# Optimization experiments

Hardware: AMD Instinct MI355X
Metric: run time of the kernel (lower is better)

The kernel has to match this reference:

```python
import jax, jax.numpy as jnp
import numpy as np

# Dims: P patterns, L pattern length, D word dim, V vocab, H mlp hidden, C classes, N doc length
P, L, D, V, H, C, N = 256, 6, 300, 100000, 256, 5, 4096


def setup_inputs() -> dict:
    key = jax.random.key(0)
    ks = jax.random.split(key, 10)
    doc = jax.random.randint(ks[0], (N,), 0, V)
    emb = jax.random.normal(ks[1], (V, D), dtype=jnp.float32)
    diags = jax.random.normal(ks[2], (P * 2 * L, D), dtype=jnp.float32)
    diags = diags / jnp.linalg.norm(diags, axis=1, keepdims=True)  # normalize() at init
    bias = jax.random.normal(ks[3], (P * 2 * L, 1), dtype=jnp.float32)
    epsilon = jax.random.normal(ks[4], (P, L - 1), dtype=jnp.float32)
    w0 = jax.random.normal(ks[5], (H, P), dtype=jnp.float32) * 0.05
    b0 = jnp.zeros((H,), jnp.float32)
    w1 = jax.random.normal(ks[6], (H, H), dtype=jnp.float32) * 0.05
    b1 = jnp.zeros((H,), jnp.float32)
    w2 = jax.random.normal(ks[7], (C, H), dtype=jnp.float32) * 0.05
    b2 = jnp.zeros((C,), jnp.float32)
    return dict(doc=doc, emb=emb, diags=diags, bias=bias, epsilon=epsilon,
                w0=w0, b0=b0, w1=w1, b1=b1, w2=w2, b2=b2)


def reference(doc, emb, diags, bias, epsilon, w0, b0, w1, b1, w2, b2):
    # fixed scalar gates: epsilon_scale = self_loop_scale = 0.5 (non-trainable)
    sls = jax.nn.sigmoid(jnp.float32(0.5))
    eps_val = jax.nn.sigmoid(jnp.float32(0.5)) * jax.nn.sigmoid(epsilon)  # [P, L-1]

    # precompute all per-token transition matrices in one GEMM
    x = emb[doc]                                                # [N, D]
    T = jax.nn.sigmoid(x @ diags.T + bias[:, 0])                # [N, P*2*L]
    T = T.reshape(-1, P, 2, L)                                  # [N, P, 2, L]

    h0 = jnp.zeros((P, L), jnp.float32).at[:, 0].set(1.0)
    zero_pad = jnp.zeros((P, 1), jnp.float32)
    one_pad = jnp.ones((P, 1), jnp.float32)

    def step(h, Tt):  # transition_once, fused over tokens via scan
        main = jnp.concatenate([zero_pad, h[:, :-1] * Tt[:, 1, :-1]], axis=1) \
               + sls * h * Tt[:, 0, :]
        h2 = main + jnp.concatenate([one_pad, main[:, :-1] * eps_val], axis=1)
        return h2, h2[:, -1]

    _, last_states = jax.lax.scan(step, h0, T)                  # last_states: [N, P]
    scores = last_states.sum(axis=0)                            # [P]

    # MLP (num_mlp_layers=2 hidden ReLU layers, then linear to classes)
    z = scores[None, :]                                         # [1, P]
    z = jax.nn.relu(z @ w0.T + b0)
    z = jax.nn.relu(z @ w1.T + b1)
    return z @ w2.T + b2                                        # [1, C]
```

## Files before the change

kernel.cpp:

```cpp
#include <hip/hip_runtime.h>
#include <hip/hip_bf16.h>
#include <cstdint>
#include <cstddef>

#define P_ 256
#define L_ 6
#define D_ 300
#define J_ 3072
#define N_ 4096
#define H_ 256
#define C_ 5
#define KP 320
#define KSTEPS 10

#define SLS 0.62245933120185459f

typedef __attribute__((ext_vector_type(8))) short short8v;
typedef __attribute__((ext_vector_type(4))) short short4v;
typedef __attribute__((ext_vector_type(4))) float f32x4;

__device__ __forceinline__ float sigmoidf_(float x) { return 1.0f / (1.0f + __expf(-x)); }
__device__ __forceinline__ float bf2f(short s) { return __uint_as_float(((unsigned)(unsigned short)s) << 16); }

__global__ __launch_bounds__(256) void prep_XB(
    const int* __restrict__ doc, const float* __restrict__ emb,
    const float* __restrict__ diags,
    __hip_bfloat16* __restrict__ X, __hip_bfloat16* __restrict__ Bb)
{
    const int i = blockIdx.x * 256 + threadIdx.x;
    const int NX = N_ * KP;
    if (i < NX) {
        const int n = i / KP, k = i - n * KP;
        float v = (k < D_) ? emb[(size_t)doc[n] * D_ + k] : 0.0f;
        X[i] = __float2bfloat16(v);
    } else {
        const int ii = i - NX;
        const int j = ii / KP, k = ii - j * KP;
        float v = (k < D_) ? diags[(size_t)j * D_ + k] : 0.0f;
        Bb[ii] = __float2bfloat16(v);
    }
}

__global__ __launch_bounds__(256) void gemm_mfma(
    const __hip_bfloat16* __restrict__ X, const __hip_bfloat16* __restrict__ Bb,
    const float* __restrict__ bias, __hip_bfloat16* __restrict__ Tt)
{
    __shared__ __hip_bfloat16 As[2][128 * 32];
    __shared__ __hip_bfloat16 Bs[2][128 * 32];

    const int tid  = threadIdx.x;
    const int lane = tid & 63;
    const int w    = tid >> 6;
    const int wr   = w >> 1, wc = w & 1;

    const int bid = blockIdx.x;
    const int swz = (bid & 7) * 96 + (bid >> 3);
    const int bx  = swz % 24, by = swz / 24;
    const int m0  = by * 128;
    const int j0  = bx * 128;

    const int srow = w * 32 + (lane >> 2);
    const int scol = (lane & 3) * 8;

    f32x4 acc[4][4];
    #pragma unroll
    for (int m = 0; m < 4; ++m)
        #pragma unroll
        for (int n = 0; n < 4; ++n)
            acc[m][n] = (f32x4){0.f, 0.f, 0.f, 0.f};

    const int fr = lane & 15;
    const int kg = (lane >> 4) * 8;

    auto stage = [&](int kt, int b) {
        const int k0 = kt * 32;
        #pragma unroll
        for (int q = 0; q < 2; ++q) {
            const __hip_bfloat16* ga = X + (size_t)(m0 + srow + q * 16) * KP + k0 + scol;
            __builtin_amdgcn_global_load_lds(
                (const __attribute__((address_space(1))) unsigned*)ga,
                (__attribute__((address_space(3))) unsigned*)(&As[b][(w * 2 + q) * 512]),
                16, 0, 0);
            const __hip_bfloat16* gb = Bb + (size_t)(j0 + srow + q * 16) * KP + k0 + scol;
            __builtin_amdgcn_global_load_lds(
                (const __attribute__((address_space(1))) unsigned*)gb,
                (__attribute__((address_space(3))) unsigned*)(&Bs[b][(w * 2 + q) * 512]),
                16, 0, 0);
        }
    };

    stage(0, 0);
    __syncthreads();

    int buf = 0;
    for (int kt = 0; kt < KSTEPS; ++kt) {
        if (kt + 1 < KSTEPS) stage(kt + 1, buf ^ 1);

        short8v a[4], b[4];
        #pragma unroll
        for (int m = 0; m < 4; ++m)
            a[m] = *(const short8v*)(&As[buf][(wr * 64 + m * 16 + fr) * 32 + kg]);
        #pragma unroll
        for (int n = 0; n < 4; ++n)
            b[n] = *(const short8v*)(&Bs[buf][(wc * 64 + n * 16 + fr) * 32 + kg]);
        #pragma unroll
        for (int m = 0; m < 4; ++m)
            #pragma unroll
            for (int n = 0; n < 4; ++n)
                acc[m][n] = __builtin_amdgcn_mfma_f32_16x16x32_bf16(a[m], b[n], acc[m][n], 0, 0, 0);

        __syncthreads();
        buf ^= 1;
    }

    #pragma unroll
    for (int n = 0; n < 4; ++n) {
        const int j = j0 + wc * 64 + n * 16 + fr;
        const float bj = bias[j];
        #pragma unroll
        for (int m = 0; m < 4; ++m) {
            const int rbase = m0 + wr * 64 + m * 16 + (lane >> 4) * 4;
            short4v pk;
            #pragma unroll
            for (int r = 0; r < 4; ++r) {
                float v = acc[m][n][r] + bj;
                __hip_bfloat16 hb = __float2bfloat16(sigmoidf_(v));
                pk[r] = *reinterpret_cast<const short*>(&hb);
            }
            *(short4v*)(Tt + (size_t)j * N_ + rbase) = pk;
        }
    }
}

__device__ __forceinline__ void compose_maps(const float* C, const float* R, float* N)
{
    #pragma unroll
    for (int j = 0; j < 7; ++j) {
        #pragma unroll
        for (int i = 0; i < 6; ++i) {
            float a = (j == 6) ? C[42 + i] : 0.0f;
            #pragma unroll
            for (int u = 0; u < 6; ++u) a = fmaf(C[u * 7 + i], R[j * 7 + u], a);
            N[j * 7 + i] = a;
        }
        float sa = R[j * 7 + 6] + ((j == 6) ? C[48] : 0.0f);
        #pragma unroll
        for (int u = 0; u < 6; ++u) sa = fmaf(C[u * 7 + 6], R[j * 7 + u], sa);
        N[j * 7 + 6] = sa;
    }
}

__global__ __launch_bounds__(256) void scan_tree(
    const __hip_bfloat16* __restrict__ Tt, const float* __restrict__ epsilon,
    float* __restrict__ scores)
{
    __shared__ float lds[256 * 49];
    const int tid = threadIdx.x;
    const int p   = blockIdx.x;

    {
        const int c = tid;
        float ep[5];
        #pragma unroll
        for (int l = 0; l < 5; ++l)
            ep[l] = SLS * (1.0f / (1.0f + __expf(-epsilon[p * 5 + l])));

        float hc[7][6], sc[7];
        #pragma unroll
        for (int j = 0; j < 7; ++j) {
            sc[j] = 0.0f;
            #pragma unroll
            for (int i = 0; i < 6; ++i) hc[j][i] = (i == j) ? 1.0f : 0.0f;
        }

        #pragma unroll
        for (int h = 0; h < 2; ++h) {
            short8v v[12];
            #pragma unroll
            for (int l = 0; l < 12; ++l)
                v[l] = *(const short8v*)(Tt + (size_t)(p * 12 + l) * N_ + c * 16 + h * 8);

            #pragma unroll
            for (int tt = 0; tt < 8; ++tt) {
                float sT0[6], T1v[6];
                #pragma unroll
                for (int l = 0; l < 6; ++l) {
                    sT0[l] = SLS * bf2f(v[l][tt]);
                    T1v[l] = bf2f(v[6 + l][tt]);
                }
                #pragma unroll
                for (int j = 0; j < 7; ++j) {
                    float m[6];
                    m[0] = hc[j][0] * sT0[0];
                    #pragma unroll
                    for (int i = 1; i < 6; ++i)
                        m[i] = fmaf(hc[j][i - 1], T1v[i - 1], hc[j][i] * sT0[i]);
                    hc[j][0] = m[0] + ((j == 6) ? 1.0f : 0.0f);
                    #pragma unroll
                    for (int i = 1; i < 6; ++i)
                        hc[j][i] = fmaf(m[i - 1], ep[i - 1], m[i]);
                    sc[j] += hc[j][5];
                }
            }
        }

        #pragma unroll
        for (int j = 0; j < 7; ++j) {
            #pragma unroll
            for (int i = 0; i < 6; ++i) lds[c * 49 + j * 7 + i] = hc[j][i];
            lds[c * 49 + j * 7 + 6] = sc[j];
        }
    }

    for (int act = 128; act >= 1; act >>= 1) {
        __syncthreads();
        float Nn[49];
        const bool on = (tid < act);
        if (on) compose_maps(&lds[(2 * tid + 1) * 49], &lds[(2 * tid) * 49], Nn);
        __syncthreads();
        if (on) {
            #pragma unroll
            for (int q = 0; q < 49; ++q) lds[tid * 49 + q] = Nn[q];
        }
    }

    if (tid == 0) scores[p] = lds[6] + lds[48];
}

__global__ __launch_bounds__(256) void mlp_head(
    const float* __restrict__ scores,
    const float* __restrict__ w0, const float* __restrict__ b0,
    const float* __restrict__ w1, const float* __restrict__ b1,
    const float* __restrict__ w2, const float* __restrict__ b2,
    float* __restrict__ out)
{
    __shared__ float s0[H_], z0[H_], z1[H_];
    const int tid = threadIdx.x;

    s0[tid] = scores[tid];
    __syncthreads();

    float acc = b0[tid];
    {
        const float4* wr = (const float4*)(w0 + (size_t)tid * P_);
        #pragma unroll 4
        for (int q = 0; q < P_ / 4; ++q) {
            float4 w = wr[q];
            acc = fmaf(w.x, s0[q * 4 + 0], acc);
            acc = fmaf(w.y, s0[q * 4 + 1], acc);
            acc = fmaf(w.z, s0[q * 4 + 2], acc);
            acc = fmaf(w.w, s0[q * 4 + 3], acc);
        }
    }
    z0[tid] = fmaxf(acc, 0.0f);
    __syncthreads();

    acc = b1[tid];
    {
        const float4* wr = (const float4*)(w1 + (size_t)tid * H_);
        #pragma unroll 4
        for (int q = 0; q < H_ / 4; ++q) {
            float4 w = wr[q];
            acc = fmaf(w.x, z0[q * 4 + 0], acc);
            acc = fmaf(w.y, z0[q * 4 + 1], acc);
            acc = fmaf(w.z, z0[q * 4 + 2], acc);
            acc = fmaf(w.w, z0[q * 4 + 3], acc);
        }
    }
    z1[tid] = fmaxf(acc, 0.0f);
    __syncthreads();

    if (tid < C_) {
        float o = b2[tid];
        const float* wr = w2 + (size_t)tid * H_;
        for (int hh = 0; hh < H_; ++hh) o = fmaf(wr[hh], z1[hh], o);
        out[tid] = o;
    }
}

extern "C" void kernel_launch(void* const* d_in, const int* in_sizes, int n_in,
                              void* d_out, int out_size, void* d_ws, size_t ws_size,
                              hipStream_t stream)
{
    const int*   doc     = (const int*)d_in[0];
    const float* emb     = (const float*)d_in[1];
    const float* diags   = (const float*)d_in[2];
    const float* bias    = (const float*)d_in[3];
    const float* epsilon = (const float*)d_in[4];
    const float* w0      = (const float*)d_in[5];
    const float* b0      = (const float*)d_in[6];
    const float* w1      = (const float*)d_in[7];
    const float* b1      = (const float*)d_in[8];
    const float* w2      = (const float*)d_in[9];
    const float* b2      = (const float*)d_in[10];
    float* out = (float*)d_out;

    float* scores = (float*)d_ws;
    __hip_bfloat16* Tt = (__hip_bfloat16*)((float*)d_ws + 256);
    __hip_bfloat16* X  = Tt + (size_t)J_ * N_;
    __hip_bfloat16* Bb = X  + (size_t)N_ * KP;

    prep_XB<<<(N_ * KP + J_ * KP) / 256, 256, 0, stream>>>(doc, emb, diags, X, Bb);
    gemm_mfma<<<(J_ / 128) * (N_ / 128), 256, 0, stream>>>(X, Bb, bias, Tt);
    scan_tree<<<P_, 256, 0, stream>>>(Tt, epsilon, scores);
    mlp_head<<<1, 256, 0, stream>>>(scores, w0, b0, w1, b1, w2, b2, out);
}
```

Measured before the change: 66.03 us.

## Fuse embedding gather and bf16 conversion into the GEMM kernel

Removes the separate prep kernel that gathered embeddings and converted emb/diags to padded bf16 buffers. The GEMM now loads fp32 rows directly from the gathered embeddings and from diags, converts them in registers and writes them to LDS, with register prefetch of the next k-step overlapping the MFMA work. This drops a kernel launch and a global write/read round trip of the bf16 operands. In exchange each tile reloads fp32 data, twice the bytes of bf16, with redundant gathers across column tiles, and the async global-to-LDS loads are replaced by register staging.

Measured after the change: 91.30 us. 1.38x slower.

```diff
diff --git a/kernel.cpp b/kernel.cpp
--- a/kernel.cpp
+++ b/kernel.cpp
@@ -10,7 +10,6 @@
 #define N_ 4096
 #define H_ 256
 #define C_ 5
-#define KP 320
 #define KSTEPS 10
 
 #define SLS 0.62245933120185459f
@@ -21,29 +20,15 @@
 
 __device__ __forceinline__ float sigmoidf_(float x) { return 1.0f / (1.0f + __expf(-x)); }
 __device__ __forceinline__ float bf2f(short s) { return __uint_as_float(((unsigned)(unsigned short)s) << 16); }
-
-__global__ __launch_bounds__(256) void prep_XB(
+__device__ __forceinline__ short f2bf(float f) {
+    __hip_bfloat16 h = __float2bfloat16(f);
+    return *reinterpret_cast<const short*>(&h);
+}
+
+__global__ __launch_bounds__(256) void gemm_fused(
     const int* __restrict__ doc, const float* __restrict__ emb,
-    const float* __restrict__ diags,
-    __hip_bfloat16* __restrict__ X, __hip_bfloat16* __restrict__ Bb)
-{
-    const int i = blockIdx.x * 256 + threadIdx.x;
-    const int NX = N_ * KP;
-    if (i < NX) {
-        const int n = i / KP, k = i - n * KP;
-        float v = (k < D_) ? emb[(size_t)doc[n] * D_ + k] : 0.0f;
-        X[i] = __float2bfloat16(v);
-    } else {
-        const int ii = i - NX;
-        const int j = ii / KP, k = ii - j * KP;
-        float v = (k < D_) ? diags[(size_t)j * D_ + k] : 0.0f;
-        Bb[ii] = __float2bfloat16(v);
-    }
-}
-
-__global__ __launch_bounds__(256) void gemm_mfma(
-    const __hip_bfloat16* __restrict__ X, const __hip_bfloat16* __restrict__ Bb,
-    const float* __restrict__ bias, __hip_bfloat16* __restrict__ Tt)
+    const float* __restrict__ diags, const float* __restrict__ bias,
+    __hip_bfloat16* __restrict__ Tt)
 {
     __shared__ __hip_bfloat16 As[2][128 * 32];
     __shared__ __hip_bfloat16 Bs[2][128 * 32];
@@ -59,8 +44,44 @@
     const int m0  = by * 128;
     const int j0  = bx * 128;
 
-    const int srow = w * 32 + (lane >> 2);
-    const int scol = (lane & 3) * 8;
+    const int r  = tid >> 1;
+    const int hf = tid & 1;
+    const float* rowA = emb   + (size_t)doc[m0 + r] * D_ + hf * 16;
+    const float* rowB = diags + (size_t)(j0 + r)   * D_ + hf * 16;
+
+    float4 av[4], bv[4];
+    auto load_step = [&](int kt) {
+        if (kt < KSTEPS - 1) {
+            const float4* pa = (const float4*)(rowA + kt * 32);
+            const float4* pb = (const float4*)(rowB + kt * 32);
+            #pragma unroll
+            for (int q = 0; q < 4; ++q) { av[q] = pa[q]; bv[q] = pb[q]; }
+        } else {
+            float* a = reinterpret_cast<float*>(av);
+            float* b = reinterpret_cast<float*>(bv);
+            #pragma unroll
+            for (int e = 0; e < 16; ++e) {
+                const int gk = 288 + hf * 16 + e;
+                const bool ok = (gk < D_);
+                a[e] = ok ? rowA[(KSTEPS - 1) * 32 + e] : 0.0f;
+                b[e] = ok ? rowB[(KSTEPS - 1) * 32 + e] : 0.0f;
+            }
+        }
+    };
+    auto store_step = [&](int b) {
+        const float* a = reinterpret_cast<const float*>(av);
+        const float* bb = reinterpret_cast<const float*>(bv);
+        short8v p0, p1, q0, q1;
+        #pragma unroll
+        for (int e = 0; e < 8; ++e) {
+            p0[e] = f2bf(a[e]);      p1[e] = f2bf(a[e + 8]);
+            q0[e] = f2bf(bb[e]);     q1[e] = f2bf(bb[e + 8]);
+        }
+        __hip_bfloat16* da = &As[b][r * 32 + hf * 16];
+        __hip_bfloat16* db = &Bs[b][r * 32 + hf * 16];
+        *(short8v*)da = p0; *(short8v*)(da + 8) = p1;
+        *(short8v*)db = q0; *(short8v*)(db + 8) = q1;
+    };
 
     f32x4 acc[4][4];
     #pragma unroll
@@ -72,45 +93,30 @@
     const int fr = lane & 15;
     const int kg = (lane >> 4) * 8;
 
-    auto stage = [&](int kt, int b) {
-        const int k0 = kt * 32;
-        #pragma unroll
-        for (int q = 0; q < 2; ++q) {
-            const __hip_bfloat16* ga = X + (size_t)(m0 + srow + q * 16) * KP + k0 + scol;
-            __builtin_amdgcn_global_load_lds(
-                (const __attribute__((address_space(1))) unsigned*)ga,
-                (__attribute__((address_space(3))) unsigned*)(&As[b][(w * 2 + q) * 512]),
-                16, 0, 0);
-            const __hip_bfloat16* gb = Bb + (size_t)(j0 + srow + q * 16) * KP + k0 + scol;
-            __builtin_amdgcn_global_load_lds(
-                (const __attribute__((address_space(1))) unsigned*)gb,
-                (__attribute__((address_space(3))) unsigned*)(&Bs[b][(w * 2 + q) * 512]),
-                16, 0, 0);
-        }
-    };
-
-    stage(0, 0);
+    load_step(0);
+    store_step(0);
     __syncthreads();
 
-    int buf = 0;
+    int cur = 0;
     for (int kt = 0; kt < KSTEPS; ++kt) {
-        if (kt + 1 < KSTEPS) stage(kt + 1, buf ^ 1);
+        if (kt + 1 < KSTEPS) load_step(kt + 1);
 
         short8v a[4], b[4];
         #pragma unroll
         for (int m = 0; m < 4; ++m)
-            a[m] = *(const short8v*)(&As[buf][(wr * 64 + m * 16 + fr) * 32 + kg]);
+            a[m] = *(const short8v*)(&As[cur][(wr * 64 + m * 16 + fr) * 32 + kg]);
         #pragma unroll
         for (int n = 0; n < 4; ++n)
-            b[n] = *(const short8v*)(&Bs[buf][(wc * 64 + n * 16 + fr) * 32 + kg]);
+            b[n] = *(const short8v*)(&Bs[cur][(wc * 64 + n * 16 + fr) * 32 + kg]);
         #pragma unroll
         for (int m = 0; m < 4; ++m)
             #pragma unroll
             for (int n = 0; n < 4; ++n)
                 acc[m][n] = __builtin_amdgcn_mfma_f32_16x16x32_bf16(a[m], b[n], acc[m][n], 0, 0, 0);
 
+        if (kt + 1 < KSTEPS) store_step(cur ^ 1);
         __syncthreads();
-        buf ^= 1;
+        cur ^= 1;
     }
 
     #pragma unroll
@@ -122,11 +128,8 @@
             const int rbase = m0 + wr * 64 + m * 16 + (lane >> 4) * 4;
             short4v pk;
             #pragma unroll
-            for (int r = 0; r < 4; ++r) {
-                float v = acc[m][n][r] + bj;
-                __hip_bfloat16 hb = __float2bfloat16(sigmoidf_(v));
-                pk[r] = *reinterpret_cast<const short*>(&hb);
-            }
+            for (int rr = 0; rr < 4; ++rr)
+                pk[rr] = f2bf(sigmoidf_(acc[m][n][rr] + bj));
             *(short4v*)(Tt + (size_t)j * N_ + rbase) = pk;
         }
     }
@@ -296,12 +299,9 @@
     float* out = (float*)d_out;
 
     float* scores = (float*)d_ws;
-    __hip_bfloat16* Tt = (__hip_bfloat16*)((float*)d_ws + 256);
-    __hip_bfloat16* X  = Tt + (size_t)J_ * N_;
-    __hip_bfloat16* Bb = X  + (size_t)N_ * KP;
-
-    prep_XB<<<(N_ * KP + J_ * KP) / 256, 256, 0, stream>>>(doc, emb, diags, X, Bb);
-    gemm_mfma<<<(J_ / 128) * (N_ / 128), 256, 0, stream>>>(X, Bb, bias, Tt);
+    __hip_bfloat16* Tt = (__hip_bfloat16*)((float*)d_ws + 512);
+
+    gemm_fused<<<(J_ / 128) * (N_ / 128), 256, 0, stream>>>(doc, emb, diags, bias, Tt);
     scan_tree<<<P_, 256, 0, stream>>>(Tt, epsilon, scores);
     mlp_head<<<1, 256, 0, stream>>>(scores, w0, b0, w1, b1, w2, b2, out);
 }
```
